# Kernel tuning notes

Measured on AMD Instinct MI355X. Metric: run time of the kernel, lower is better.

## Reference

```python
import jax, jax.numpy as jnp
import numpy as np


def conv1x1(x, w, b):
    # x: (b,c,h,w), w: (o,c), b: (o,)
    return jnp.einsum('oc,bchw->bohw', w, x) + b[None, :, None, None]


def make_grid(b, h, w, outH, outW, scale, offset):
    # Replicates the torch grid construction (align_corners=True style normalization).
    gx = ((jnp.arange(outW, dtype=jnp.float32) + 0.5) / scale - 0.5) * 2.0 / (w - 1) - 1.0
    gy = ((jnp.arange(outH, dtype=jnp.float32) + 0.5) / scale - 0.5) * 2.0 / (h - 1) - 1.0
    ix = jnp.broadcast_to(gx[None, None, :], (b, outH, outW))
    iy = jnp.broadcast_to(gy[None, :, None], (b, outH, outW))
    if offset is not None:
        ix = ix + offset[:, 0] * 2.0 / (w - 1)
        iy = iy + offset[:, 1] * 2.0 / (h - 1)
    return ix, iy


def grid_sample_zeros(img, ix, iy):
    # Bilinear grid_sample, padding_mode='zeros', align_corners=False (torch default).
    b, c, h, w = img.shape
    fx = ((ix + 1.0) * w - 1.0) / 2.0
    fy = ((iy + 1.0) * h - 1.0) / 2.0
    x0 = jnp.floor(fx); y0 = jnp.floor(fy)
    x1 = x0 + 1.0; y1 = y0 + 1.0
    wx1 = fx - x0; wx0 = 1.0 - wx1
    wy1 = fy - y0; wy0 = 1.0 - wy1
    bidx = jnp.arange(b)[:, None, None]

    def gather(xc, yc):
        valid = (xc >= 0) & (xc <= w - 1) & (yc >= 0) & (yc <= h - 1)
        xi = jnp.clip(xc, 0, w - 1).astype(jnp.int32)
        yi = jnp.clip(yc, 0, h - 1).astype(jnp.int32)
        v = img[bidx, :, yi, xi]  # (b,H,W,c)
        return jnp.where(valid[..., None], v, 0.0)

    out = (gather(x0, y0) * (wx0 * wy0)[..., None]
           + gather(x1, y0) * (wx1 * wy0)[..., None]
           + gather(x0, y1) * (wx0 * wy1)[..., None]
           + gather(x1, y1) * (wx1 * wy1)[..., None])
    return jnp.transpose(out, (0, 3, 1, 2))  # (b,c,H,W)


def setup_inputs() -> dict:
    key = jax.random.key(0)
    C, E = 64, 4
    ks = jax.random.split(key, 12)
    s = 0.05
    return {
        'x': jax.random.normal(ks[0], (2, C, 128, 128), dtype=jnp.float32),
        'weight_compress': jax.random.normal(ks[1], (E, C // 8, C), dtype=jnp.float32) * s,
        'weight_expand': jax.random.normal(ks[2], (E, C, C // 8), dtype=jnp.float32) * s,
        'w1': jax.random.normal(ks[3], (C, C + 4), dtype=jnp.float32) * s,
        'b1': jax.random.normal(ks[4], (C,), dtype=jnp.float32) * s,
        'w2': jax.random.normal(ks[5], (C, C), dtype=jnp.float32) * s,
        'b2': jax.random.normal(ks[6], (C,), dtype=jnp.float32) * s,
        'wr': jax.random.normal(ks[7], (E, C), dtype=jnp.float32) * s,
        'br': jax.random.normal(ks[8], (E,), dtype=jnp.float32) * s,
        'wo': jax.random.normal(ks[9], (2, C), dtype=jnp.float32) * s,
        'bo': jax.random.normal(ks[10], (2,), dtype=jnp.float32) * s,
        'scale': 2,
        'outH': 256,
        'outW': 256,
    }


def reference(x, weight_compress, weight_expand, w1, b1, w2, b2, wr, br, wo, bo, scale, outH, outW):
    b, c, h, w = x.shape
    # relative sub-pixel coordinates
    ah = jnp.arange(outH, dtype=jnp.float32)
    aw = jnp.arange(outW, dtype=jnp.float32)
    coor_h = (ah + 0.5) / scale - jnp.floor((ah + 0.5) / scale + 0.001) - 0.5  # (outH,)
    coor_w = (aw + 0.5) / scale - jnp.floor((aw + 0.5) / scale + 0.001) - 0.5  # (outW,)
    ones_hw = jnp.full((outH, outW), 1.0 / scale, dtype=jnp.float32)
    coords = jnp.stack([ones_hw, ones_hw,
                        jnp.broadcast_to(coor_h[:, None], (outH, outW)),
                        jnp.broadcast_to(coor_w[None, :], (outH, outW))], axis=0)  # (4,H,W)
    coords = jnp.broadcast_to(coords[None], (b, 4, outH, outW))

    ix, iy = make_grid(b, h, w, outH, outW, scale, None)
    pre_fea = grid_sample_zeros(x, ix, iy)  # (b,C,H,W)

    inp = jnp.concatenate([coords, pre_fea], axis=1)  # (b,C+4,H,W)
    emb = jax.nn.relu(conv1x1(jax.nn.relu(conv1x1(inp, w1, b1)), w2, b2))

    offset = conv1x1(emb, wo, bo)  # (b,2,H,W)
    ix2, iy2 = make_grid(b, h, w, outH, outW, scale, offset)
    fea0 = grid_sample_zeros(x, ix2, iy2)  # (b,C,H,W)

    r = jax.nn.sigmoid(conv1x1(emb, wr, br))  # (b,E,H,W) routing weights
    # per-pixel expert-blended compress->expand (algebraically identical to
    # materializing per-pixel weight matrices, but as E small GEMM pairs)
    comp = jnp.einsum('behw,edc,bchw->bdhw', r, weight_compress, fea0)  # (b,C/8,H,W)
    out = jnp.einsum('behw,ecd,bdhw->bchw', r, weight_expand, comp)    # (b,C,H,W)
    return out + fea0
```

## Files before the change

### kernel.cpp

```cpp
#include <hip/hip_runtime.h>
#include <math.h>

#define BATCH 2
#define C 64
#define HIN 128
#define WIN 128
#define HW (HIN * WIN)
#define OH 256
#define OW 256

#define BLK 256
#define PIX 64
#define SC 16
#define ASTR 72


typedef __attribute__((ext_vector_type(8))) short bf16x8;
typedef __attribute__((ext_vector_type(4))) float f32x4;

__device__ __forceinline__ unsigned short f2bf(float f) {
    unsigned u = __float_as_uint(f);
    u += 0x7FFFu + ((u >> 16) & 1u);
    return (unsigned short)(u >> 16);
}
__device__ __forceinline__ float bf2f(unsigned short s) {
    return __uint_as_float(((unsigned)s) << 16);
}

__device__ __forceinline__ void bilin_setup(float gx, float gy,
    int& i00, int& i10, int& i01, int& i11,
    float& w00, float& w10, float& w01, float& w11)
{
    const float fx = ((gx + 1.0f) * WIN - 1.0f) * 0.5f;
    const float fy = ((gy + 1.0f) * HIN - 1.0f) * 0.5f;
    const float x0 = floorf(fx), y0 = floorf(fy);
    const float wx1 = fx - x0, wx0 = 1.0f - wx1;
    const float wy1 = fy - y0, wy0 = 1.0f - wy1;
    const float x1 = x0 + 1.0f, y1 = y0 + 1.0f;
    const bool vx0 = (x0 >= 0.0f) && (x0 <= (float)(WIN - 1));
    const bool vx1 = (x1 >= 0.0f) && (x1 <= (float)(WIN - 1));
    const bool vy0 = (y0 >= 0.0f) && (y0 <= (float)(HIN - 1));
    const bool vy1 = (y1 >= 0.0f) && (y1 <= (float)(HIN - 1));
    const int xi0 = (int)fminf(fmaxf(x0, 0.0f), (float)(WIN - 1));
    const int xi1 = (int)fminf(fmaxf(x1, 0.0f), (float)(WIN - 1));
    const int yi0 = (int)fminf(fmaxf(y0, 0.0f), (float)(HIN - 1));
    const int yi1 = (int)fminf(fmaxf(y1, 0.0f), (float)(HIN - 1));
    w00 = wx0 * wy0 * ((vx0 && vy0) ? 1.0f : 0.0f);
    w10 = wx1 * wy0 * ((vx1 && vy0) ? 1.0f : 0.0f);
    w01 = wx0 * wy1 * ((vx0 && vy1) ? 1.0f : 0.0f);
    w11 = wx1 * wy1 * ((vx1 && vy1) ? 1.0f : 0.0f);
    i00 = yi0 * WIN + xi0;  i10 = yi0 * WIN + xi1;
    i01 = yi1 * WIN + xi0;  i11 = yi1 * WIN + xi1;
}

__global__ __launch_bounds__(BLK, 4) void scab_kernel(
    const float* __restrict__ x,
    const float* __restrict__ wcm,
    const float* __restrict__ wex,
    const float* __restrict__ w1,
    const float* __restrict__ b1,
    const float* __restrict__ w2,
    const float* __restrict__ b2,
    const float* __restrict__ wr,
    const float* __restrict__ br,
    const float* __restrict__ wo,
    const float* __restrict__ bo,
    float* __restrict__ out)
{
    __shared__ __align__(16) short act[PIX * ASTR];
    __shared__ float red[8 * BLK];

    const int tid  = threadIdx.x;
    const int lane = tid & 63;
    const int s    = __builtin_amdgcn_readfirstlane(tid >> 6);
    const int cb   = s * SC;
    const int l15  = lane & 15;
    const int quad = lane >> 4;
    const int nn   = cb + l15;

    const int gp = blockIdx.x * PIX + lane;
    const int ox = gp & (OW - 1);
    const int oy = (gp >> 8) & (OH - 1);
    const int bb = gp >> 16;

    const float gx = ((ox + 0.5f) * 0.5f - 0.5f) * (2.0f / (WIN - 1)) - 1.0f;
    const float gy = ((oy + 0.5f) * 0.5f - 0.5f) * (2.0f / (HIN - 1)) - 1.0f;

    const float* __restrict__ xb = x + bb * (C * HW);

    bf16x8 bw1[2], bw2[2];
    #pragma unroll
    for (int ks = 0; ks < 2; ++ks) {
        const float* __restrict__ s1p = w1 + nn * (C + 4) + 4 + ks * 32 + quad * 8;
        const float* __restrict__ s2p = w2 + nn * C + ks * 32 + quad * 8;
        #pragma unroll
        for (int j = 0; j < 8; ++j) {
            bw1[ks][j] = (short)f2bf(s1p[j]);
            bw2[ks][j] = (short)f2bf(s2p[j]);
        }
    }

    {
        int i00, i10, i01, i11;
        float w00, w10, w01, w11;
        bilin_setup(gx, gy, i00, i10, i01, i11, w00, w10, w01, w11);
        bf16x8 v0, v1;
        #pragma unroll
        for (int kk = 0; kk < SC; kk += 4) {
            float l[16];
            #pragma unroll
            for (int k = 0; k < 4; ++k) {
                const float* __restrict__ xc = xb + (cb + kk + k) * HW;
                l[4*k+0] = xc[i00]; l[4*k+1] = xc[i10];
                l[4*k+2] = xc[i01]; l[4*k+3] = xc[i11];
            }
            #pragma unroll
            for (int k = 0; k < 4; ++k) {
                const float pf = l[4*k]*w00 + l[4*k+1]*w10 + l[4*k+2]*w01 + l[4*k+3]*w11;
                const short b = (short)f2bf(pf);
                if (kk + k < 8) v0[kk + k] = b; else v1[kk + k - 8] = b;
            }
        }
        *(bf16x8*)&act[lane * ASTR + cb]     = v0;
        *(bf16x8*)&act[lane * ASTR + cb + 8] = v1;
    }
    __syncthreads();

    const float coor_h = (oy & 1) ? 0.25f : -0.25f;
    f32x4 acc[4];
    {
        const float4 wh = *(const float4*)(w1 + nn * (C + 4));
        const float qn = b1[nn] + (wh.x + wh.y) * 0.5f + wh.z * coor_h;
        const float e0 = qn - 0.25f * wh.w;
        const float e1 = qn + 0.25f * wh.w;
        #pragma unroll
        for (int t = 0; t < 4; ++t) acc[t] = (f32x4){e0, e1, e0, e1};
    }
    #pragma unroll
    for (int t = 0; t < 4; ++t) {
        #pragma unroll
        for (int ks = 0; ks < 2; ++ks) {
            const bf16x8 af = *(const bf16x8*)&act[(t*16 + l15) * ASTR + ks*32 + quad*8];
            acc[t] = __builtin_amdgcn_mfma_f32_16x16x32_bf16(af, bw1[ks], acc[t], 0, 0, 0);
        }
    }
    __syncthreads();
    #pragma unroll
    for (int t = 0; t < 4; ++t)
        #pragma unroll
        for (int r = 0; r < 4; ++r)
            act[(t*16 + quad*4 + r) * ASTR + nn] = (short)f2bf(fmaxf(acc[t][r], 0.0f));
    __syncthreads();

    {
        const float b2n = b2[nn];
        #pragma unroll
        for (int t = 0; t < 4; ++t) acc[t] = (f32x4){b2n, b2n, b2n, b2n};
    }
    #pragma unroll
    for (int t = 0; t < 4; ++t) {
        #pragma unroll
        for (int ks = 0; ks < 2; ++ks) {
            const bf16x8 af = *(const bf16x8*)&act[(t*16 + l15) * ASTR + ks*32 + quad*8];
            acc[t] = __builtin_amdgcn_mfma_f32_16x16x32_bf16(af, bw2[ks], acc[t], 0, 0, 0);
        }
    }
    __syncthreads();
    #pragma unroll
    for (int t = 0; t < 4; ++t)
        #pragma unroll
        for (int r = 0; r < 4; ++r)
            act[(t*16 + quad*4 + r) * ASTR + nn] = (short)f2bf(fmaxf(acc[t][r], 0.0f));
    __syncthreads();

    float hx = 0.0f, hy = 0.0f, z0p = 0.0f, z1p = 0.0f, z2p = 0.0f, z3p = 0.0f;
    {
        const bf16x8 u0 = *(const bf16x8*)&act[lane * ASTR + cb];
        const bf16x8 u1 = *(const bf16x8*)&act[lane * ASTR + cb + 8];
        float em[SC];
        #pragma unroll
        for (int k = 0; k < 8; ++k) {
            em[k]     = bf2f((unsigned short)u0[k]);
            em[8 + k] = bf2f((unsigned short)u1[k]);
        }
        #pragma unroll
        for (int k = 0; k < SC; ++k) {
            const int o = cb + k;
            const float e = em[k];
            hx  = fmaf(wo[o],         e, hx);
            hy  = fmaf(wo[C + o],     e, hy);
            z0p = fmaf(wr[o],         e, z0p);
            z1p = fmaf(wr[C + o],     e, z1p);
            z2p = fmaf(wr[2 * C + o], e, z2p);
            z3p = fmaf(wr[3 * C + o], e, z3p);
        }
    }
    red[0 * 256 + s * 64 + lane] = hx;
    red[1 * 256 + s * 64 + lane] = hy;
    red[2 * 256 + s * 64 + lane] = z0p;
    red[3 * 256 + s * 64 + lane] = z1p;
    red[4 * 256 + s * 64 + lane] = z2p;
    red[5 * 256 + s * 64 + lane] = z3p;
    __syncthreads();

    float offx = bo[0], offy = bo[1];
    float z0 = br[0], z1 = br[1], z2 = br[2], z3 = br[3];
    #pragma unroll
    for (int ss = 0; ss < 4; ++ss) {
        offx += red[0 * 256 + ss * 64 + lane];
        offy += red[1 * 256 + ss * 64 + lane];
        z0   += red[2 * 256 + ss * 64 + lane];
        z1   += red[3 * 256 + ss * 64 + lane];
        z2   += red[4 * 256 + ss * 64 + lane];
        z3   += red[5 * 256 + ss * 64 + lane];
    }
    const float rg0 = 1.0f / (1.0f + __expf(-z0));
    const float rg1 = 1.0f / (1.0f + __expf(-z1));
    const float rg2 = 1.0f / (1.0f + __expf(-z2));
    const float rg3 = 1.0f / (1.0f + __expf(-z3));
    __syncthreads();

    float f[SC];
    float cp[8];
    #pragma unroll
    for (int d = 0; d < 8; ++d) cp[d] = 0.0f;
    {
        int j00, j10, j01, j11;
        float v00, v10, v01, v11;
        bilin_setup(gx + offx * (2.0f / (WIN - 1)),
                    gy + offy * (2.0f / (HIN - 1)),
                    j00, j10, j01, j11, v00, v10, v01, v11);
        #pragma unroll
        for (int kk = 0; kk < SC; kk += 4) {
            float l[16];
            #pragma unroll
            for (int k = 0; k < 4; ++k) {
                const float* __restrict__ xc = xb + (cb + kk + k) * HW;
                l[4*k+0] = xc[j00]; l[4*k+1] = xc[j10];
                l[4*k+2] = xc[j01]; l[4*k+3] = xc[j11];
            }
            #pragma unroll
            for (int k = 0; k < 4; ++k) {
                const float fc = l[4*k]*v00 + l[4*k+1]*v10 + l[4*k+2]*v01 + l[4*k+3]*v11;
                f[kk + k] = fc;
                const int c = cb + kk + k;
                const float s0 = rg0 * fc, s1 = rg1 * fc, s2 = rg2 * fc, s3 = rg3 * fc;
                #pragma unroll
                for (int d = 0; d < 8; ++d) {
                    cp[d] = fmaf(wcm[(0 * 8 + d) * C + c], s0, cp[d]);
                    cp[d] = fmaf(wcm[(1 * 8 + d) * C + c], s1, cp[d]);
                    cp[d] = fmaf(wcm[(2 * 8 + d) * C + c], s2, cp[d]);
                    cp[d] = fmaf(wcm[(3 * 8 + d) * C + c], s3, cp[d]);
                }
            }
        }
    }
    #pragma unroll
    for (int d = 0; d < 8; ++d) red[d * 256 + s * 64 + lane] = cp[d];
    __syncthreads();

    float comp[8];
    #pragma unroll
    for (int d = 0; d < 8; ++d) {
        float v = red[d * 256 + 0 * 64 + lane];
        v += red[d * 256 + 1 * 64 + lane];
        v += red[d * 256 + 2 * 64 + lane];
        v += red[d * 256 + 3 * 64 + lane];
        comp[d] = v;
    }

    float* __restrict__ ob = out + bb * (C * OH * OW) + oy * OW + ox;
    #pragma unroll
    for (int k = 0; k < SC; ++k) {
        const int c = cb + k;
        const float* __restrict__ we0 = wex + (0 * C + c) * 8;
        const float* __restrict__ we1 = wex + (1 * C + c) * 8;
        const float* __restrict__ we2 = wex + (2 * C + c) * 8;
        const float* __restrict__ we3 = wex + (3 * C + c) * 8;
        float s0 = 0.0f, s1 = 0.0f, s2 = 0.0f, s3 = 0.0f;
        #pragma unroll
        for (int d = 0; d < 8; ++d) {
            s0 = fmaf(we0[d], comp[d], s0);
            s1 = fmaf(we1[d], comp[d], s1);
            s2 = fmaf(we2[d], comp[d], s2);
            s3 = fmaf(we3[d], comp[d], s3);
        }
        float acc2 = f[k];
        acc2 = fmaf(rg0, s0, acc2);
        acc2 = fmaf(rg1, s1, acc2);
        acc2 = fmaf(rg2, s2, acc2);
        acc2 = fmaf(rg3, s3, acc2);
        ob[c * (OH * OW)] = acc2;
    }
}

extern "C" void kernel_launch(void* const* d_in, const int* in_sizes, int n_in,
                              void* d_out, int out_size, void* d_ws, size_t ws_size,
                              hipStream_t stream) {
    const float* x   = (const float*)d_in[0];
    const float* wcm = (const float*)d_in[1];
    const float* wex = (const float*)d_in[2];
    const float* w1  = (const float*)d_in[3];
    const float* b1  = (const float*)d_in[4];
    const float* w2  = (const float*)d_in[5];
    const float* b2  = (const float*)d_in[6];
    const float* wr  = (const float*)d_in[7];
    const float* br  = (const float*)d_in[8];
    const float* wo  = (const float*)d_in[9];
    const float* bo  = (const float*)d_in[10];
    float* out = (float*)d_out;

    const int total  = BATCH * OH * OW;
    const int blocks = total / PIX;
    scab_kernel<<<blocks, BLK, 0, stream>>>(x, wcm, wex, w1, b1, w2, b2,
                                            wr, br, wo, bo, out);
}
```

Baseline: 124.9 us.

## Move expert compress/expand mixing onto bf16 MFMA via shared-memory staging

Replaces the per-thread scalar FMA loops for the routed compress (64→8 per expert) and expand (8→64 per expert) with bf16 MFMA tiles. Sampled features are written to LDS as bf16 and multiplied by all four experts' compress weights in one GEMM, then blended with the routing weights. The routed compress result is rescaled per expert, staged in LDS and fed to a single K=32 expand MFMA. This removes many scalar FMAs and the partial-sum reduction, but adds extra LDS round trips and barriers, and drops the compress/expand path from fp32 to bf16 precision.

```diff
diff --git a/kernel.cpp b/kernel.cpp
--- a/kernel.cpp
+++ b/kernel.cpp
@@ -13,6 +13,8 @@
 #define PIX 64
 #define SC 16
 #define ASTR 72
+#define YSTR 36
+#define OSTR 68
 
 
 typedef __attribute__((ext_vector_type(8))) short bf16x8;
@@ -68,7 +70,7 @@
     float* __restrict__ out)
 {
     __shared__ __align__(16) short act[PIX * ASTR];
-    __shared__ float red[8 * BLK];
+    __shared__ __align__(16) float red[PIX * OSTR];
 
     const int tid  = threadIdx.x;
     const int lane = tid & 63;
@@ -88,16 +90,25 @@
 
     const float* __restrict__ xb = x + bb * (C * HW);
 
-    bf16x8 bw1[2], bw2[2];
-    #pragma unroll
-    for (int ks = 0; ks < 2; ++ks) {
-        const float* __restrict__ s1p = w1 + nn * (C + 4) + 4 + ks * 32 + quad * 8;
-        const float* __restrict__ s2p = w2 + nn * C + ks * 32 + quad * 8;
-        #pragma unroll
-        for (int j = 0; j < 8; ++j) {
-            bw1[ks][j] = (short)f2bf(s1p[j]);
-            bw2[ks][j] = (short)f2bf(s2p[j]);
-        }
+    bf16x8 bw1[2], bw2[2], bwc[2], bwe;
+    {
+        const int nt1  = s & 1;
+        const int eo_g = nt1 * 16 + l15;
+        #pragma unroll
+        for (int ks = 0; ks < 2; ++ks) {
+            const float* __restrict__ s1p = w1 + nn * (C + 4) + 4 + ks * 32 + quad * 8;
+            const float* __restrict__ s2p = w2 + nn * C + ks * 32 + quad * 8;
+            const float* __restrict__ scp = wcm + eo_g * C + ks * 32 + quad * 8;
+            #pragma unroll
+            for (int j = 0; j < 8; ++j) {
+                bw1[ks][j] = (short)f2bf(s1p[j]);
+                bw2[ks][j] = (short)f2bf(s2p[j]);
+                bwc[ks][j] = (short)f2bf(scp[j]);
+            }
+        }
+        const float* __restrict__ sep = wex + (quad * C + nn) * 8;
+        #pragma unroll
+        for (int j = 0; j < 8; ++j) bwe[j] = (short)f2bf(sep[j]);
     }
 
     {
@@ -177,16 +188,10 @@
     {
         const bf16x8 u0 = *(const bf16x8*)&act[lane * ASTR + cb];
         const bf16x8 u1 = *(const bf16x8*)&act[lane * ASTR + cb + 8];
-        float em[SC];
-        #pragma unroll
-        for (int k = 0; k < 8; ++k) {
-            em[k]     = bf2f((unsigned short)u0[k]);
-            em[8 + k] = bf2f((unsigned short)u1[k]);
-        }
         #pragma unroll
         for (int k = 0; k < SC; ++k) {
             const int o = cb + k;
-            const float e = em[k];
+            const float e = bf2f((unsigned short)(k < 8 ? u0[k] : u1[k - 8]));
             hx  = fmaf(wo[o],         e, hx);
             hy  = fmaf(wo[C + o],     e, hy);
             z0p = fmaf(wr[o],         e, z0p);
@@ -218,18 +223,15 @@
     const float rg1 = 1.0f / (1.0f + __expf(-z1));
     const float rg2 = 1.0f / (1.0f + __expf(-z2));
     const float rg3 = 1.0f / (1.0f + __expf(-z3));
-    __syncthreads();
 
     float f[SC];
-    float cp[8];
-    #pragma unroll
-    for (int d = 0; d < 8; ++d) cp[d] = 0.0f;
     {
         int j00, j10, j01, j11;
         float v00, v10, v01, v11;
         bilin_setup(gx + offx * (2.0f / (WIN - 1)),
                     gy + offy * (2.0f / (HIN - 1)),
                     j00, j10, j01, j11, v00, v10, v01, v11);
+        bf16x8 v0, v1;
         #pragma unroll
         for (int kk = 0; kk < SC; kk += 4) {
             float l[16];
@@ -243,54 +245,81 @@
             for (int k = 0; k < 4; ++k) {
                 const float fc = l[4*k]*v00 + l[4*k+1]*v10 + l[4*k+2]*v01 + l[4*k+3]*v11;
                 f[kk + k] = fc;
-                const int c = cb + kk + k;
-                const float s0 = rg0 * fc, s1 = rg1 * fc, s2 = rg2 * fc, s3 = rg3 * fc;
-                #pragma unroll
-                for (int d = 0; d < 8; ++d) {
-                    cp[d] = fmaf(wcm[(0 * 8 + d) * C + c], s0, cp[d]);
-                    cp[d] = fmaf(wcm[(1 * 8 + d) * C + c], s1, cp[d]);
-                    cp[d] = fmaf(wcm[(2 * 8 + d) * C + c], s2, cp[d]);
-                    cp[d] = fmaf(wcm[(3 * 8 + d) * C + c], s3, cp[d]);
-                }
-            }
-        }
-    }
-    #pragma unroll
-    for (int d = 0; d < 8; ++d) red[d * 256 + s * 64 + lane] = cp[d];
-    __syncthreads();
-
-    float comp[8];
-    #pragma unroll
-    for (int d = 0; d < 8; ++d) {
-        float v = red[d * 256 + 0 * 64 + lane];
-        v += red[d * 256 + 1 * 64 + lane];
-        v += red[d * 256 + 2 * 64 + lane];
-        v += red[d * 256 + 3 * 64 + lane];
-        comp[d] = v;
-    }
+                const short b = (short)f2bf(fc);
+                if (kk + k < 8) v0[kk + k] = b; else v1[kk + k - 8] = b;
+            }
+        }
+        *(bf16x8*)&act[lane * ASTR + cb]     = v0;
+        *(bf16x8*)&act[lane * ASTR + cb + 8] = v1;
+    }
+    __syncthreads();
+
+    {
+        const int nt1 = s & 1;
+        const int mb  = (s >> 1) * 2;
+        #pragma unroll
+        for (int mi = 0; mi < 2; ++mi) {
+            const int mt = mb + mi;
+            f32x4 yac = (f32x4){0.0f, 0.0f, 0.0f, 0.0f};
+            #pragma unroll
+            for (int ks = 0; ks < 2; ++ks) {
+                const bf16x8 af = *(const bf16x8*)&act[(mt*16 + l15) * ASTR + ks*32 + quad*8];
+                yac = __builtin_amdgcn_mfma_f32_16x16x32_bf16(af, bwc[ks], yac, 0, 0, 0);
+            }
+            #pragma unroll
+            for (int r = 0; r < 4; ++r)
+                red[(mt*16 + quad*4 + r) * YSTR + nt1*16 + l15] = yac[r];
+        }
+    }
+    __syncthreads();
+
+    {
+        float comp[8];
+        const float* __restrict__ yr = &red[lane * YSTR];
+        #pragma unroll
+        for (int d = 0; d < 8; ++d) {
+            float v = rg0 * yr[d];
+            v = fmaf(rg1, yr[8 + d],  v);
+            v = fmaf(rg2, yr[16 + d], v);
+            v = fmaf(rg3, yr[24 + d], v);
+            comp[d] = v;
+        }
+        bf16x8 t0, t1, t2, t3;
+        #pragma unroll
+        for (int d = 0; d < 8; ++d) {
+            t0[d] = (short)f2bf(rg0 * comp[d]);
+            t1[d] = (short)f2bf(rg1 * comp[d]);
+            t2[d] = (short)f2bf(rg2 * comp[d]);
+            t3[d] = (short)f2bf(rg3 * comp[d]);
+        }
+        __syncthreads();
+        *(bf16x8*)&act[lane * ASTR + 0]  = t0;
+        *(bf16x8*)&act[lane * ASTR + 8]  = t1;
+        *(bf16x8*)&act[lane * ASTR + 16] = t2;
+        *(bf16x8*)&act[lane * ASTR + 24] = t3;
+    }
+    __syncthreads();
+
+    #pragma unroll
+    for (int t = 0; t < 4; ++t) {
+        f32x4 oac = (f32x4){0.0f, 0.0f, 0.0f, 0.0f};
+        const bf16x8 af = *(const bf16x8*)&act[(t*16 + l15) * ASTR + quad*8];
+        oac = __builtin_amdgcn_mfma_f32_16x16x32_bf16(af, bwe, oac, 0, 0, 0);
+        #pragma unroll
+        for (int r = 0; r < 4; ++r)
+            red[(t*16 + quad*4 + r) * OSTR + nn] = oac[r];
+    }
+    __syncthreads();
 
     float* __restrict__ ob = out + bb * (C * OH * OW) + oy * OW + ox;
-    #pragma unroll
-    for (int k = 0; k < SC; ++k) {
-        const int c = cb + k;
-        const float* __restrict__ we0 = wex + (0 * C + c) * 8;
-        const float* __restrict__ we1 = wex + (1 * C + c) * 8;
-        const float* __restrict__ we2 = wex + (2 * C + c) * 8;
-        const float* __restrict__ we3 = wex + (3 * C + c) * 8;
-        float s0 = 0.0f, s1 = 0.0f, s2 = 0.0f, s3 = 0.0f;
-        #pragma unroll
-        for (int d = 0; d < 8; ++d) {
-            s0 = fmaf(we0[d], comp[d], s0);
-            s1 = fmaf(we1[d], comp[d], s1);
-            s2 = fmaf(we2[d], comp[d], s2);
-            s3 = fmaf(we3[d], comp[d], s3);
-        }
-        float acc2 = f[k];
-        acc2 = fmaf(rg0, s0, acc2);
-        acc2 = fmaf(rg1, s1, acc2);
-        acc2 = fmaf(rg2, s2, acc2);
-        acc2 = fmaf(rg3, s3, acc2);
-        ob[c * (OH * OW)] = acc2;
+    const float* __restrict__ orow = &red[lane * OSTR + cb];
+    #pragma unroll
+    for (int kk = 0; kk < SC; kk += 4) {
+        const float4 e4 = *(const float4*)(orow + kk);
+        ob[(cb + kk + 0) * (OH * OW)] = f[kk + 0] + e4.x;
+        ob[(cb + kk + 1) * (OH * OW)] = f[kk + 1] + e4.y;
+        ob[(cb + kk + 2) * (OH * OW)] = f[kk + 2] + e4.z;
+        ob[(cb + kk + 3) * (OH * OW)] = f[kk + 3] + e4.w;
     }
 }
 
```

Measured after the change: 119.3 us. -4.5%, faster.
